# Kernel tuning notes

Measured on AMD Instinct MI355X. Metric: run time of the kernel, lower is better.

Reference implementation:

```python
import jax, jax.numpy as jnp
import numpy as np

DEPTH, DIM, DFF, DT, VOCAB = 3, 512, 2048, 64, 32000
B, L = 2, 512


def setup_inputs() -> dict:
    key = jax.random.key(0)
    ks = jax.random.split(key, 16)
    z = lambda *s: jnp.zeros(s, jnp.float32)
    o = lambda *s: jnp.ones(s, jnp.float32)
    n = lambda k, s, std: jax.random.normal(k, s, jnp.float32) * std
    return {
        "x": jax.random.normal(ks[0], (B, L, VOCAB), jnp.float32),
        "tok_in_w": n(ks[1], (DIM, VOCAB), VOCAB ** -0.5),
        "tok_in_b": z(DIM),
        "ln1_g": o(DEPTH, DIM), "ln1_b": z(DEPTH, DIM),
        "fc_w": n(ks[2], (DEPTH, DT, DIM), DIM ** -0.5), "fc_b": z(DEPTH, DT),
        "tin_w": n(ks[3], (DEPTH, DT, DIM), DIM ** -0.5), "tin_b": z(DEPTH, DT),
        "a_w": n(ks[4], (DEPTH, 2 * DT, DT), DT ** -0.5),
        "h0": jax.random.normal(ks[5], (DEPTH, DT, 2), jnp.float32),
        "tout_w": n(ks[6], (DEPTH, DIM, DT), DT ** -0.5), "tout_b": z(DEPTH, DIM),
        "ln2_g": o(DEPTH, DIM), "ln2_b": z(DEPTH, DIM),
        "ffn_w1": n(ks[7], (DEPTH, DFF, DIM), DIM ** -0.5), "ffn_b1": z(DEPTH, DFF),
        "ffn_w2": n(ks[8], (DEPTH, DIM, DFF), DFF ** -0.5), "ffn_b2": z(DEPTH, DIM),
        "lnf_g": o(DIM), "lnf_b": z(DIM),
        "tok_out_w": n(ks[9], (VOCAB, DIM), DIM ** -0.5), "tok_out_b": z(VOCAB),
    }


def _ln(x, g, b, eps=1e-5):
    m = x.mean(-1, keepdims=True)
    v = jnp.mean((x - m) ** 2, -1, keepdims=True)
    return (x - m) * jax.lax.rsqrt(v + eps) * g + b


def _sioconv(x, a_w, h0):
    # x: (B, L, D). Complex decaying linear recurrence, materialized as the
    # same O(L^2) kernel the torch code builds (cumsum of complex logs replaces
    # the FFT-conv-with-ones, which computes exactly a prefix sum along k).
    Bx, Lx, D = x.shape
    za = (x @ a_w.T).reshape(Bx, Lx, D, 2)
    m2 = za[..., 0] ** 2 + za[..., 1] ** 2
    scale = jax.lax.rsqrt(m2) * jnp.exp(-m2)            # |a| = exp(-|a0|^2)
    a = (za[..., 0] + 1j * za[..., 1]) * scale.astype(jnp.complex64)
    a_ln = jnp.log(a)                                   # (B, L, D)
    S = jnp.cumsum(a_ln, axis=1)
    Sp = jnp.concatenate([jnp.zeros_like(S[:, :1]), S[:, :-1]], axis=1)
    # diff[b,i,k,d] = sum_{j=i..k} a_ln[b,j,d]
    diff = S[:, None, :, :] - Sp[:, :, None, :]          # (B, i, k, D)
    idx = jnp.arange(Lx)
    mask = (idx[None, :] >= idx[:, None] - 1)[None, :, :, None]  # triu(diag=-1)
    c = jnp.where(mask, jnp.exp(jnp.where(mask, diff, 0.0)), 0.0)
    h0c = h0[:, 0] + 1j * h0[:, 1]                       # (D,) complex init state
    xc = x.astype(jnp.complex64)
    xs = jnp.concatenate([jnp.broadcast_to(h0c, (Bx, 1, D)), xc[:, :-1]], axis=1)
    h = jnp.einsum('bikd,bkd->bid', c, xs)               # (B, L, D) complex
    h = h.at[:, -1].add(xc[:, -1])
    return h.real.astype(x.dtype)


def _block(x, p):
    (g1, b1, fcw, fcb, tiw, tib, aw, h0, tow, tob, g2, b2, w1, fb1, w2, fb2) = p
    r = x
    xn = _ln(x, g1, b1)
    y = jax.nn.silu(xn @ fcw.T + fcb)                    # gate (B, L, DT)
    t = _sioconv(xn @ tiw.T + tib, aw, h0)
    x = (t * y) @ tow.T + tob + r
    r = x
    xn = _ln(x, g2, b2)
    return jax.nn.silu(xn @ w1.T + fb1) @ w2.T + fb2 + r


def reference(x, tok_in_w, tok_in_b, ln1_g, ln1_b, fc_w, fc_b, tin_w, tin_b, a_w, h0, tout_w, tout_b, ln2_g, ln2_b, ffn_w1, ffn_b1, ffn_w2, ffn_b2, lnf_g, lnf_b, tok_out_w, tok_out_b):
    h = x @ tok_in_w.T + tok_in_b
    for i in range(DEPTH):
        p = (ln1_g[i], ln1_b[i], fc_w[i], fc_b[i], tin_w[i], tin_b[i], a_w[i], h0[i],
             tout_w[i], tout_b[i], ln2_g[i], ln2_b[i], ffn_w1[i], ffn_b1[i], ffn_w2[i], ffn_b2[i])
        h = _block(h, p)
    h = _ln(h, lnf_g, lnf_b)
    return h @ tok_out_w.T + tok_out_b
```

## Files before the change

kernel.cpp:

```cpp
#include <hip/hip_runtime.h>
#include <hip/hip_bf16.h>


#define LDIM 512
#define SEQL 512
#define DT_ 64
#define NC 16
#define CL 32
#define BK 32

typedef short s16x4 __attribute__((ext_vector_type(4)));
typedef short s16x8 __attribute__((ext_vector_type(8)));
typedef float f32x4 __attribute__((ext_vector_type(4)));

__device__ __forceinline__ unsigned short f2bf(float f) {
  unsigned u = __builtin_bit_cast(unsigned, f);
  return (unsigned short)((u + 0x7fffu + ((u >> 16) & 1u)) >> 16);
}

__device__ __forceinline__ void split2(float f, short& hi, short& lo) {
  unsigned u = __builtin_bit_cast(unsigned, f);
  hi = (short)(u >> 16);
  float hf = __builtin_bit_cast(float, u & 0xFFFF0000u);
  float lf = f - hf;
  lo = (short)(__builtin_bit_cast(unsigned, lf) >> 16);
}

template <int BM, int BN, int ACT, bool RES, bool ATOM, bool BIAS, bool SPL,
          int AACT = 0, bool WBF = false>
__global__ __launch_bounds__(256) void gemm_bt(
    const float* __restrict__ A, const float* __restrict__ W,
    const float* __restrict__ bias, const float* __restrict__ R,
    float* __restrict__ C, int M, int N, int K, int kc) {
  constexpr int WM = BM / 2, WN = BN / 2, TM = WM / 16, TN = WN / 16;
  constexpr int LDA = BK + 8;
  constexpr int PLANES = SPL ? 2 : 1;
  __shared__ __align__(16) short As[BM * LDA * PLANES];
  __shared__ __align__(16) short Bs[BN * LDA * PLANES];

  const int tid = threadIdx.x;
  const int wid = tid >> 6, lane = tid & 63;
  const int q = lane >> 4, l16 = lane & 15;
  const int wm = (wid >> 1) * WM, wn = (wid & 1) * WN;
  const int m0 = blockIdx.y * BM, n0 = blockIdx.x * BN;
  const int kbeg = blockIdx.z * kc;
  const int kend = min(K, kbeg + kc);

  f32x4 acc[TM][TN] = {};

  constexpr int AF = BM * BK / 1024;
  constexpr int BF = BN * BK / 1024;

  for (int k0 = kbeg; k0 < kend; k0 += BK) {
#pragma unroll
    for (int t = 0; t < AF; t++) {
      int fi = tid + t * 256;
      int row = fi >> 3, col = (fi & 7) << 2;
      float4 v = *(const float4*)(A + (size_t)(m0 + row) * K + k0 + col);
      float* vp = (float*)&v;
      s16x4 hv, lv;
#pragma unroll
      for (int c = 0; c < 4; c++) {
        if (AACT == 1) vp[c] = vp[c] / (1.f + __expf(-vp[c]));
        if (SPL) {
          short h_, l_;
          split2(vp[c], h_, l_);
          hv[c] = h_; lv[c] = l_;
        } else {
          hv[c] = (short)f2bf(vp[c]);
        }
      }
      *(s16x4*)(&As[row * LDA + col]) = hv;
      if (SPL) *(s16x4*)(&As[BM * LDA + row * LDA + col]) = lv;
    }
    if constexpr (WBF) {
      const short* Wb = (const short*)W;
      constexpr int BF2 = BN / 64;
#pragma unroll
      for (int t = 0; t < BF2; t++) {
        int fi = tid + t * 256;
        int row = fi >> 2, col8 = (fi & 3) << 3;
        s16x8 v = *(const s16x8*)(Wb + (size_t)(n0 + row) * K + k0 + col8);
        *(s16x8*)(&Bs[row * LDA + col8]) = v;
      }
    } else {
#pragma unroll
      for (int t = 0; t < BF; t++) {
        int fi = tid + t * 256;
        int row = fi >> 3, col = (fi & 7) << 2;
        float4 v = *(const float4*)(W + (size_t)(n0 + row) * K + k0 + col);
        const float* vp = (const float*)&v;
        s16x4 hv, lv;
#pragma unroll
        for (int c = 0; c < 4; c++) {
          if (SPL) {
            short h_, l_;
            split2(vp[c], h_, l_);
            hv[c] = h_; lv[c] = l_;
          } else {
            hv[c] = (short)f2bf(vp[c]);
          }
        }
        *(s16x4*)(&Bs[row * LDA + col]) = hv;
        if (SPL) *(s16x4*)(&Bs[BN * LDA + row * LDA + col]) = lv;
      }
    }
    __syncthreads();
    s16x8 ah[TM], bh[TN], al[TM], bl[TN];
#pragma unroll
    for (int i = 0; i < TM; i++) {
      ah[i] = *(const s16x8*)(&As[(wm + i * 16 + l16) * LDA + q * 8]);
      if (SPL) al[i] = *(const s16x8*)(&As[BM * LDA + (wm + i * 16 + l16) * LDA + q * 8]);
    }
#pragma unroll
    for (int j = 0; j < TN; j++) {
      bh[j] = *(const s16x8*)(&Bs[(wn + j * 16 + l16) * LDA + q * 8]);
      if (SPL) bl[j] = *(const s16x8*)(&Bs[BN * LDA + (wn + j * 16 + l16) * LDA + q * 8]);
    }
#pragma unroll
    for (int i = 0; i < TM; i++)
#pragma unroll
      for (int j = 0; j < TN; j++) {
        acc[i][j] = __builtin_amdgcn_mfma_f32_16x16x32_bf16(ah[i], bh[j], acc[i][j], 0, 0, 0);
        if (SPL) {
          acc[i][j] = __builtin_amdgcn_mfma_f32_16x16x32_bf16(ah[i], bl[j], acc[i][j], 0, 0, 0);
          acc[i][j] = __builtin_amdgcn_mfma_f32_16x16x32_bf16(al[i], bh[j], acc[i][j], 0, 0, 0);
        }
      }
    __syncthreads();
  }

#pragma unroll
  for (int i = 0; i < TM; i++)
#pragma unroll
    for (int j = 0; j < TN; j++)
#pragma unroll
      for (int r = 0; r < 4; r++) {
        int m = m0 + wm + i * 16 + q * 4 + r;
        int n = n0 + wn + j * 16 + l16;
        float v = acc[i][j][r];
        if (BIAS && kbeg == 0) v += bias[n];
        if (ACT == 1) v = v / (1.f + __expf(-v));
        if (RES) v += R[(size_t)m * N + n];
        if (ATOM) atomicAdd(&C[(size_t)m * N + n], v);
        else C[(size_t)m * N + n] = v;
      }
}

__global__ __launch_bounds__(256) void fill0(float* __restrict__ p) {
  size_t i = (size_t)(blockIdx.x * 256 + threadIdx.x) * 4;
  *(float4*)(p + i) = make_float4(0.f, 0.f, 0.f, 0.f);
}

__global__ __launch_bounds__(256) void cvt_rne(const float* __restrict__ src,
                                               short* __restrict__ dst) {
  size_t i = (size_t)(blockIdx.x * 256 + threadIdx.x) * 4;
  float4 v = *(const float4*)(src + i);
  const float* vp = (const float*)&v;
  s16x4 o;
#pragma unroll
  for (int c = 0; c < 4; c++) o[c] = (short)f2bf(vp[c]);
  *(s16x4*)(dst + i) = o;
}

__global__ __launch_bounds__(256) void ln512(const float* __restrict__ x,
                                             const float* __restrict__ g,
                                             const float* __restrict__ b,
                                             float* __restrict__ o) {
  int wid = threadIdx.x >> 6, lane = threadIdx.x & 63;
  int row = blockIdx.x * 4 + wid;
  const float* xr = x + (size_t)row * 512 + lane * 8;
  float4 v0 = *(const float4*)xr;
  float4 v1 = *(const float4*)(xr + 4);
  float s = v0.x + v0.y + v0.z + v0.w + v1.x + v1.y + v1.z + v1.w;
  float ss = v0.x * v0.x + v0.y * v0.y + v0.z * v0.z + v0.w * v0.w +
             v1.x * v1.x + v1.y * v1.y + v1.z * v1.z + v1.w * v1.w;
#pragma unroll
  for (int m = 32; m; m >>= 1) { s += __shfl_xor(s, m); ss += __shfl_xor(ss, m); }
  float mean = s * (1.f / 512.f);
  float var = ss * (1.f / 512.f) - mean * mean;
  float rstd = rsqrtf(var + 1e-5f);
  const float* gp = g + lane * 8;
  const float* bp = b + lane * 8;
  float4 g0 = *(const float4*)gp, g1 = *(const float4*)(gp + 4);
  float4 b0 = *(const float4*)bp, b1 = *(const float4*)(bp + 4);
  float* op = o + (size_t)row * 512 + lane * 8;
  float4 r0, r1;
  r0.x = (v0.x - mean) * rstd * g0.x + b0.x;
  r0.y = (v0.y - mean) * rstd * g0.y + b0.y;
  r0.z = (v0.z - mean) * rstd * g0.z + b0.z;
  r0.w = (v0.w - mean) * rstd * g0.w + b0.w;
  r1.x = (v1.x - mean) * rstd * g1.x + b1.x;
  r1.y = (v1.y - mean) * rstd * g1.y + b1.y;
  r1.z = (v1.z - mean) * rstd * g1.z + b1.z;
  r1.w = (v1.w - mean) * rstd * g1.w + b1.w;
  *(float4*)op = r0;
  *(float4*)(op + 4) = r1;
}

__device__ __forceinline__ float2 a_of(const float* __restrict__ za, int b, int i, int d) {
  float zr = za[(size_t)(b * SEQL + i) * 128 + 2 * d];
  float zi = za[(size_t)(b * SEQL + i) * 128 + 2 * d + 1];
  float m2 = zr * zr + zi * zi;
  float sc = rsqrtf(m2) * __expf(-m2);
  return make_float2(zr * sc, zi * sc);
}

__device__ __forceinline__ float2 xsm1_of(const float* __restrict__ u,
                                          const float* __restrict__ h0,
                                          int b, int i, int d) {
  if (i == 0) return make_float2(0.f, 0.f);
  if (i == 1) return make_float2(h0[d * 2], h0[d * 2 + 1]);
  return make_float2(u[(size_t)(b * SEQL + i - 2) * DT_ + d], 0.f);
}

__global__ __launch_bounds__(1024) void scan_all(const float* __restrict__ za,
                                                 const float* __restrict__ u,
                                                 const float* __restrict__ h0,
                                                 const float* __restrict__ y,
                                                 float* __restrict__ p) {
  __shared__ float2 sA[NC * 64], sB[NC * 64], sT[NC * 64];
  const int b = blockIdx.x;
  const int t = threadIdx.x;
  const int d = t & 63, c = t >> 6;

  float2 Aa = make_float2(1.f, 0.f), Bv = make_float2(0.f, 0.f);
  for (int i = c * CL + CL - 1; i >= c * CL; i--) {
    float2 a = a_of(za, b, i, d);
    float2 xs = xsm1_of(u, h0, b, i, d);
    float2 nb, nA;
    nb.x = xs.x + a.x * Bv.x - a.y * Bv.y;
    nb.y = xs.y + a.x * Bv.y + a.y * Bv.x;
    nA.x = a.x * Aa.x - a.y * Aa.y;
    nA.y = a.x * Aa.y + a.y * Aa.x;
    Bv = nb; Aa = nA;
  }
  sA[c * 64 + d] = Aa;
  sB[c * 64 + d] = Bv;
  __syncthreads();

  if (c == 0) {
    float2 tt = make_float2(u[(size_t)(b * SEQL + SEQL - 2) * DT_ + d], 0.f);
    for (int cc = NC - 1; cc >= 0; cc--) {
      sT[cc * 64 + d] = tt;
      float2 A = sA[cc * 64 + d], Bc = sB[cc * 64 + d];
      float2 nt;
      nt.x = A.x * tt.x - A.y * tt.y + Bc.x;
      nt.y = A.x * tt.y + A.y * tt.x + Bc.y;
      tt = nt;
    }
  }
  __syncthreads();

  float2 tt = sT[c * 64 + d];
  for (int i = c * CL + CL - 1; i >= c * CL; i--) {
    float2 a = a_of(za, b, i, d);
    float2 xs = xsm1_of(u, h0, b, i, d);
    float2 nt;
    nt.x = xs.x + a.x * tt.x - a.y * tt.y;
    nt.y = xs.y + a.x * tt.y + a.y * tt.x;
    tt = nt;
    float hr = tt.x;
    if (i == SEQL - 1) hr += u[(size_t)(b * SEQL + SEQL - 1) * DT_ + d];
    size_t o = (size_t)(b * SEQL + i) * DT_ + d;
    float yv = y[o];
    yv = yv / (1.f + __expf(-yv));
    p[o] = hr * yv;
  }
}

extern "C" void kernel_launch(void* const* d_in, const int* in_sizes, int n_in,
                              void* d_out, int out_size, void* d_ws, size_t ws_size,
                              hipStream_t stream) {
  const float* x        = (const float*)d_in[0];
  const float* tok_in_w = (const float*)d_in[1];
  const float* tok_in_b = (const float*)d_in[2];
  const float* ln1_g    = (const float*)d_in[3];
  const float* ln1_b    = (const float*)d_in[4];
  const float* fc_w     = (const float*)d_in[5];
  const float* fc_b     = (const float*)d_in[6];
  const float* tin_w    = (const float*)d_in[7];
  const float* tin_b    = (const float*)d_in[8];
  const float* a_w      = (const float*)d_in[9];
  const float* h0       = (const float*)d_in[10];
  const float* tout_w   = (const float*)d_in[11];
  const float* tout_b   = (const float*)d_in[12];
  const float* ln2_g    = (const float*)d_in[13];
  const float* ln2_b    = (const float*)d_in[14];
  const float* ffn_w1   = (const float*)d_in[15];
  const float* ffn_b1   = (const float*)d_in[16];
  const float* ffn_w2   = (const float*)d_in[17];
  const float* ffn_b2   = (const float*)d_in[18];
  const float* lnf_g    = (const float*)d_in[19];
  const float* lnf_b    = (const float*)d_in[20];
  const float* tok_out_w = (const float*)d_in[21];
  const float* tok_out_b = (const float*)d_in[22];
  float* out = (float*)d_out;

  float* ws = (float*)d_ws;
  float* h  = ws;
  float* xn = h + 524288;
  float* y  = xn + 524288;
  float* u  = y + 65536;
  float* za = u + 65536;
  float* p  = za + 131072;
  float* f1 = p + 65536;
  short* wb = (short*)(f1 + 2097152);
  const bool use_wbf = ws_size >= (size_t)(3473408 + 8192000) * 4;

  dim3 blk(256);

  fill0<<<512, blk, 0, stream>>>(h);
  gemm_bt<128, 128, 0, false, true, true, true><<<dim3(4, 8, 32), blk, 0, stream>>>(
      x, tok_in_w, tok_in_b, nullptr, h, 1024, 512, 32000, 1024);

  for (int l = 0; l < 3; l++) {
    ln512<<<256, blk, 0, stream>>>(h, ln1_g + l * 512, ln1_b + l * 512, xn);
    fill0<<<128, blk, 0, stream>>>(y);
    gemm_bt<32, 64, 0, false, true, true, true><<<dim3(1, 32, 8), blk, 0, stream>>>(
        xn, fc_w + l * 32768, fc_b + l * 64, nullptr, y, 1024, 64, 512, 64);
    gemm_bt<32, 64, 0, false, true, true, true><<<dim3(1, 32, 8), blk, 0, stream>>>(
        xn, tin_w + l * 32768, tin_b + l * 64, nullptr, u, 1024, 64, 512, 64);
    gemm_bt<32, 64, 0, false, false, false, true><<<dim3(2, 32, 1), blk, 0, stream>>>(
        u, a_w + l * 8192, nullptr, nullptr, za, 1024, 128, 64, 64);
    scan_all<<<2, 1024, 0, stream>>>(za, u, h0 + l * 128, y, p);
    gemm_bt<64, 64, 0, true, false, true, true><<<dim3(8, 16, 1), blk, 0, stream>>>(
        p, tout_w + l * 32768, tout_b + l * 512, h, h, 1024, 512, 64, 64);
    ln512<<<256, blk, 0, stream>>>(h, ln2_g + l * 512, ln2_b + l * 512, xn);
    fill0<<<2048, blk, 0, stream>>>(f1);
    gemm_bt<128, 128, 0, false, true, true, true><<<dim3(16, 8, 4), blk, 0, stream>>>(
        xn, ffn_w1 + l * 1048576, ffn_b1 + l * 2048, nullptr, f1, 1024, 2048, 512, 128);
    gemm_bt<128, 128, 0, false, true, true, true, 1><<<dim3(4, 8, 16), blk, 0, stream>>>(
        f1, ffn_w2 + l * 1048576, ffn_b2 + l * 512, nullptr, h, 1024, 512, 2048, 128);
  }

  ln512<<<256, blk, 0, stream>>>(h, lnf_g, lnf_b, xn);
  if (use_wbf) {
    cvt_rne<<<16000, blk, 0, stream>>>(tok_out_w, wb);
    gemm_bt<128, 128, 0, false, false, true, false, 0, true><<<dim3(250, 8, 1), blk, 0, stream>>>(
        xn, (const float*)wb, tok_out_b, nullptr, out, 1024, 32000, 512, 512);
  } else {
    gemm_bt<128, 128, 0, false, false, true, false><<<dim3(250, 8, 1), blk, 0, stream>>>(
        xn, tok_out_w, tok_out_b, nullptr, out, 1024, 32000, 512, 512);
  }
}
```

Measured before the change: 1.118 ms.

## Swizzle input-embedding GEMM blocks, fuse fc/tin GEMMs, retune tiles and split-K

The input-embedding GEMM now runs on a 1D grid whose block index is swizzled so that the 8 M-tiles sharing a K chunk run next to each other, which should improve L2 reuse of the large weight and activation slices. The fc and tin projections are merged into one launch through a DUAL mode that picks the weight, bias and output from blockIdx.x. Tile shapes are changed for the a_w and tout GEMMs, and split-K is halved for the FFN GEMMs to cut atomic traffic at the cost of fewer blocks. Fewer launches and less atomic contention are traded for lower parallelism on the smaller GEMMs.

```diff
diff --git a/kernel.cpp b/kernel.cpp
--- a/kernel.cpp
+++ b/kernel.cpp
@@ -27,11 +27,13 @@
 }
 
 template <int BM, int BN, int ACT, bool RES, bool ATOM, bool BIAS, bool SPL,
-          int AACT = 0, bool WBF = false>
+          int AACT = 0, bool WBF = false, bool SWZ = false, bool DUAL = false>
 __global__ __launch_bounds__(256) void gemm_bt(
     const float* __restrict__ A, const float* __restrict__ W,
     const float* __restrict__ bias, const float* __restrict__ R,
-    float* __restrict__ C, int M, int N, int K, int kc) {
+    float* __restrict__ C, int M, int N, int K, int kc,
+    const float* __restrict__ W2, const float* __restrict__ bias2,
+    float* __restrict__ C2) {
   constexpr int WM = BM / 2, WN = BN / 2, TM = WM / 16, TN = WN / 16;
   constexpr int LDA = BK + 8;
   constexpr int PLANES = SPL ? 2 : 1;
@@ -42,8 +44,20 @@
   const int wid = tid >> 6, lane = tid & 63;
   const int q = lane >> 4, l16 = lane & 15;
   const int wm = (wid >> 1) * WM, wn = (wid & 1) * WN;
-  const int m0 = blockIdx.y * BM, n0 = blockIdx.x * BN;
-  const int kbeg = blockIdx.z * kc;
+
+  int bx, by, bz;
+  if constexpr (SWZ) {
+    int b = blockIdx.x;
+    by = b & 7; bx = (b >> 3) & 3; bz = b >> 5;
+  } else {
+    bx = blockIdx.x; by = blockIdx.y; bz = blockIdx.z;
+  }
+  if constexpr (DUAL) {
+    if (bx) { W = W2; bias = bias2; C = C2; }
+    bx = 0;
+  }
+  const int m0 = by * BM, n0 = bx * BN;
+  const int kbeg = bz * kc;
   const int kend = min(K, kbeg + kc);
 
   f32x4 acc[TM][TN] = {};
@@ -311,36 +325,45 @@
   dim3 blk(256);
 
   fill0<<<512, blk, 0, stream>>>(h);
-  gemm_bt<128, 128, 0, false, true, true, true><<<dim3(4, 8, 32), blk, 0, stream>>>(
-      x, tok_in_w, tok_in_b, nullptr, h, 1024, 512, 32000, 1024);
+  gemm_bt<128, 128, 0, false, true, true, true, 0, false, true>
+      <<<dim3(1024), blk, 0, stream>>>(
+      x, tok_in_w, tok_in_b, nullptr, h, 1024, 512, 32000, 1024,
+      nullptr, nullptr, nullptr);
 
   for (int l = 0; l < 3; l++) {
     ln512<<<256, blk, 0, stream>>>(h, ln1_g + l * 512, ln1_b + l * 512, xn);
     fill0<<<128, blk, 0, stream>>>(y);
-    gemm_bt<32, 64, 0, false, true, true, true><<<dim3(1, 32, 8), blk, 0, stream>>>(
-        xn, fc_w + l * 32768, fc_b + l * 64, nullptr, y, 1024, 64, 512, 64);
-    gemm_bt<32, 64, 0, false, true, true, true><<<dim3(1, 32, 8), blk, 0, stream>>>(
-        xn, tin_w + l * 32768, tin_b + l * 64, nullptr, u, 1024, 64, 512, 64);
-    gemm_bt<32, 64, 0, false, false, false, true><<<dim3(2, 32, 1), blk, 0, stream>>>(
-        u, a_w + l * 8192, nullptr, nullptr, za, 1024, 128, 64, 64);
+    gemm_bt<64, 64, 0, false, true, true, true, 0, false, false, true>
+        <<<dim3(2, 16, 4), blk, 0, stream>>>(
+        xn, fc_w + l * 32768, fc_b + l * 64, nullptr, y, 1024, 64, 512, 128,
+        tin_w + l * 32768, tin_b + l * 64, u);
+    gemm_bt<64, 64, 0, false, false, false, true><<<dim3(2, 16, 1), blk, 0, stream>>>(
+        u, a_w + l * 8192, nullptr, nullptr, za, 1024, 128, 64, 64,
+        nullptr, nullptr, nullptr);
     scan_all<<<2, 1024, 0, stream>>>(za, u, h0 + l * 128, y, p);
-    gemm_bt<64, 64, 0, true, false, true, true><<<dim3(8, 16, 1), blk, 0, stream>>>(
-        p, tout_w + l * 32768, tout_b + l * 512, h, h, 1024, 512, 64, 64);
+    gemm_bt<64, 128, 0, true, false, true, true><<<dim3(4, 16, 1), blk, 0, stream>>>(
+        p, tout_w + l * 32768, tout_b + l * 512, h, h, 1024, 512, 64, 64,
+        nullptr, nullptr, nullptr);
     ln512<<<256, blk, 0, stream>>>(h, ln2_g + l * 512, ln2_b + l * 512, xn);
     fill0<<<2048, blk, 0, stream>>>(f1);
-    gemm_bt<128, 128, 0, false, true, true, true><<<dim3(16, 8, 4), blk, 0, stream>>>(
-        xn, ffn_w1 + l * 1048576, ffn_b1 + l * 2048, nullptr, f1, 1024, 2048, 512, 128);
-    gemm_bt<128, 128, 0, false, true, true, true, 1><<<dim3(4, 8, 16), blk, 0, stream>>>(
-        f1, ffn_w2 + l * 1048576, ffn_b2 + l * 512, nullptr, h, 1024, 512, 2048, 128);
+    gemm_bt<128, 128, 0, false, true, true, true><<<dim3(16, 8, 2), blk, 0, stream>>>(
+        xn, ffn_w1 + l * 1048576, ffn_b1 + l * 2048, nullptr, f1, 1024, 2048, 512, 256,
+        nullptr, nullptr, nullptr);
+    gemm_bt<128, 128, 0, false, true, true, true, 1><<<dim3(4, 8, 8), blk, 0, stream>>>(
+        f1, ffn_w2 + l * 1048576, ffn_b2 + l * 512, nullptr, h, 1024, 512, 2048, 256,
+        nullptr, nullptr, nullptr);
   }
 
   ln512<<<256, blk, 0, stream>>>(h, lnf_g, lnf_b, xn);
   if (use_wbf) {
     cvt_rne<<<16000, blk, 0, stream>>>(tok_out_w, wb);
-    gemm_bt<128, 128, 0, false, false, true, false, 0, true><<<dim3(250, 8, 1), blk, 0, stream>>>(
-        xn, (const float*)wb, tok_out_b, nullptr, out, 1024, 32000, 512, 512);
+    gemm_bt<128, 128, 0, false, false, true, false, 0, true>
+        <<<dim3(250, 8, 1), blk, 0, stream>>>(
+        xn, (const float*)wb, tok_out_b, nullptr, out, 1024, 32000, 512, 512,
+        nullptr, nullptr, nullptr);
   } else {
     gemm_bt<128, 128, 0, false, false, true, false><<<dim3(250, 8, 1), blk, 0, stream>>>(
-        xn, tok_out_w, tok_out_b, nullptr, out, 1024, 32000, 512, 512);
-  }
-}
+        xn, tok_out_w, tok_out_b, nullptr, out, 1024, 32000, 512, 512,
+        nullptr, nullptr, nullptr);
+  }
+}
```

Result: no change. 1.114 ms (-0.3%).
